# Performance work log

Measured on AMD Instinct MI355X. Metric: run time of the kernel, lower is better.

Reference implementation:

```python
import jax, jax.numpy as jnp
import numpy as np

N_NODES = 10000
N_EDGES = 160000
BATCH = 32
IN_FEAT = 64
POLY_K = 5
OUT_FEAT = 128


def setup_inputs() -> dict:
    key = jax.random.key(0)
    k_x, k_r, k_c, k_v, k_w, k_b = jax.random.split(key, 6)
    x = jax.random.normal(k_x, (BATCH, N_NODES, IN_FEAT), dtype=jnp.float32)
    lap_rows = jax.random.randint(k_r, (N_EDGES,), 0, N_NODES, dtype=jnp.int32)
    lap_cols = jax.random.randint(k_c, (N_EDGES,), 0, N_NODES, dtype=jnp.int32)
    # small values keep the degree-5 Chebyshev recurrence numerically tame
    lap_vals = jax.random.normal(k_v, (N_EDGES,), dtype=jnp.float32) * 0.05
    weight = jax.random.normal(k_w, (IN_FEAT * POLY_K, OUT_FEAT), dtype=jnp.float32) * 0.1
    bias = jax.random.normal(k_b, (1, 1, OUT_FEAT), dtype=jnp.float32) * 0.1
    return {"x": x, "lap_rows": lap_rows, "lap_cols": lap_cols,
            "lap_vals": lap_vals, "weight": weight, "bias": bias,
            "pooling_size": 4}


def _spmm(rows, cols, vals, m):
    # sparse [N,N] @ dense [N,M] via gather + segment_sum
    return jax.ops.segment_sum(vals[:, None] * m[cols], rows, num_segments=N_NODES)


def reference(x, lap_rows, lap_cols, lap_vals, weight, bias, pooling_size):
    B, N, F = x.shape
    K = POLY_K
    Fo = weight.shape[1]
    # x0: [N, F*B]
    x0 = jnp.transpose(x, (1, 2, 0)).reshape(N, F * B)
    terms = [x0]
    if K > 1:
        x1 = _spmm(lap_rows, lap_cols, lap_vals, x0)
        terms.append(x1)
        for _ in range(2, K):
            x2 = 2.0 * _spmm(lap_rows, lap_cols, lap_vals, x1) - x0
            terms.append(x2)
            x0, x1 = x1, x2
    xk = jnp.stack(terms, axis=0)                      # [K, N, F*B]
    xk = xk.reshape(K, N, F, B)
    xk = jnp.transpose(xk, (3, 1, 2, 0))               # [B, N, F, K]
    xk = xk.reshape(B * N, F * K)
    out = (xk @ weight).reshape(B, N, Fo)              # dense projection
    out = jax.nn.relu(out + bias)                      # bias + ReLU
    if pooling_size > 1:
        out = out.reshape(B, N // pooling_size, pooling_size, Fo).max(axis=2)
    return out
```

## Files before the change

### kernel.cpp

```cpp
#include <hip/hip_runtime.h>
#include <hip/hip_bf16.h>
#include <cstddef>
#include <cstdint>

#define N_NODES 10000
#define N_EDGES 160000
#define BATCH 32
#define IN_FEAT 64
#define POLY_K 5
#define OUT_FEAT 128
#define KTOT 320
#define POOLSZ 4
#define NPOOL 2500
#define NSL 16

typedef short bf16x8 __attribute__((ext_vector_type(8)));
typedef unsigned short u16x8 __attribute__((ext_vector_type(8)));
typedef unsigned int u32x4 __attribute__((ext_vector_type(4)));
typedef float f32x4 __attribute__((ext_vector_type(4)));
typedef float f32x2 __attribute__((ext_vector_type(2)));

__device__ __forceinline__ unsigned short f2bf(float f) {
  unsigned int u = __float_as_uint(f);
  unsigned int r = u + 0x7FFFu + ((u >> 16) & 1u);
  return (unsigned short)(r >> 16);
}
__device__ __forceinline__ float bf2f(unsigned short u) {
  return __uint_as_float(((unsigned int)u) << 16);
}
__device__ __forceinline__ f32x2 unpk(unsigned int u) {
  f32x2 r;
  r[0] = __uint_as_float(u << 16);
  r[1] = __uint_as_float(u & 0xFFFF0000u);
  return r;
}


__global__ void zero_int_kernel(int* __restrict__ p, int n) {
  int i = blockIdx.x * 256 + threadIdx.x;
  if (i < n) p[i] = 0;
}

__global__ void hist_kernel(const int* __restrict__ rows, int* __restrict__ deg) {
  int e = blockIdx.x * 256 + threadIdx.x;
  if (e < N_EDGES) atomicAdd(&deg[rows[e]], 1);
}

__global__ void scan_kernel(const int* __restrict__ deg, int* __restrict__ row_start,
                            int* __restrict__ cursor) {
  __shared__ int wsum[16];
  __shared__ int carry_sm;
  int t = threadIdx.x;
  int lane = t & 63, wid = t >> 6;
  if (t == 0) { carry_sm = 0; row_start[0] = 0; }
  __syncthreads();
  for (int base = 0; base < N_NODES; base += 1024) {
    int idx = base + t;
    int v = (idx < N_NODES) ? deg[idx] : 0;
    int x = v;
    #pragma unroll
    for (int off = 1; off < 64; off <<= 1) {
      int y = __shfl_up(x, off, 64);
      if (lane >= off) x += y;
    }
    if (lane == 63) wsum[wid] = x;
    __syncthreads();
    if (wid == 0) {
      int sv = (lane < 16) ? wsum[lane] : 0;
      #pragma unroll
      for (int off = 1; off < 16; off <<= 1) {
        int y = __shfl_up(sv, off, 64);
        if (lane >= off) sv += y;
      }
      if (lane < 16) wsum[lane] = sv;
    }
    __syncthreads();
    int incl = x + (wid > 0 ? wsum[wid - 1] : 0) + carry_sm;
    if (idx < N_NODES) {
      row_start[idx + 1] = incl;
      cursor[idx] = incl - v;
    }
    __syncthreads();
    if (t == 1023) carry_sm = incl;
    __syncthreads();
  }
}

__global__ void scatter_kernel(const int* __restrict__ rows, const int* __restrict__ cols,
                               const float* __restrict__ vals, int* __restrict__ cursor,
                               int* __restrict__ csr_cols, float* __restrict__ csr_vals) {
  int e = blockIdx.x * 256 + threadIdx.x;
  if (e < N_EDGES) {
    int r = rows[e];
    int p = atomicAdd(&cursor[r], 1);
    csr_cols[p] = cols[e];
    csr_vals[p] = vals[e];
  }
}


__global__ void wpack_kernel(const float* __restrict__ weight, unsigned short* __restrict__ wpack) {
  int id = blockIdx.x * 256 + threadIdx.x;
  if (id >= 5120) return;
  int ft = id / 640;
  int c = (id / 64) % 10;
  int l = id % 64;
  int fo = ft * 16 + (l & 15);
  unsigned short v[8];
  #pragma unroll
  for (int j = 0; j < 8; ++j) {
    int k = c * 32 + ((l >> 4)) * 8 + j;
    int row = (k & 63) * POLY_K + (k >> 6);
    v[j] = f2bf(weight[row * OUT_FEAT + fo]);
  }
  ushort4* dst = (ushort4*)&wpack[(size_t)id * 8];
  dst[0] = make_ushort4(v[0], v[1], v[2], v[3]);
  dst[1] = make_ushort4(v[4], v[5], v[6], v[7]);
}


template <int BB>
__global__ __launch_bounds__(256) void transpose_kernel(const float* __restrict__ x,
                                                        unsigned short* __restrict__ t0, int b0) {
  constexpr int CB = 64 * BB;
  constexpr int SCOLS = CB / NSL;
  constexpr size_t SLICE_SL = (size_t)N_NODES * SCOLS;
  int n = blockIdx.x;
  int t = threadIdx.x;
  for (int i = t * 8; i < CB; i += 2048) {
    int b = i >> 6;
    int f = i & 63;
    const float* xp = &x[((size_t)(b0 + b) * N_NODES + n) * IN_FEAT + f];
    float4 v0 = *(const float4*)xp;
    float4 v1 = *(const float4*)(xp + 4);
    u16x8 o;
    o[0] = f2bf(v0.x); o[1] = f2bf(v0.y); o[2] = f2bf(v0.z); o[3] = f2bf(v0.w);
    o[4] = f2bf(v1.x); o[5] = f2bf(v1.y); o[6] = f2bf(v1.z); o[7] = f2bf(v1.w);
    int sl = i / SCOLS;
    int cw = i & (SCOLS - 1);
    *(u16x8*)&t0[(size_t)sl * SLICE_SL + (size_t)n * SCOLS + cw] = o;
  }
}


template <int BB>
__global__ __launch_bounds__(256) void spmm_kernel(const unsigned short* __restrict__ xin,
                                                   const unsigned short* __restrict__ prev,
                                                   unsigned short* __restrict__ xout,
                                                   const int* __restrict__ row_start,
                                                   const int* __restrict__ csr_cols,
                                                   const float* __restrict__ csr_vals,
                                                   float alpha, int use_prev) {
  constexpr int CB = 64 * BB;
  constexpr int SCOLS = CB / NSL;
  constexpr size_t SLICE_SL = (size_t)N_NODES * SCOLS;
  constexpr int LPR = SCOLS / 8;
  constexpr int RPB = 256 / LPR;
  constexpr int RB = (N_NODES + RPB - 1) / RPB;
  constexpr int PHB = RB * 8;
  int bid = blockIdx.x;
  int phase = bid / PHB;
  int rem = bid - phase * PHB;
  int xcd = rem & 7;
  int rowblk = rem >> 3;
  int slice = phase * 8 + xcd;
  int t = threadIdx.x;
  int rl = t / LPR;
  int cl = t - rl * LPR;
  int n = rowblk * RPB + rl;
  if (n >= N_NODES) return;
  unsigned off = (unsigned)cl * 8u;

  const unsigned short* xs = xin  + (size_t)slice * SLICE_SL;
  const unsigned short* ps = prev + (size_t)slice * SLICE_SL;
  unsigned short*       os = xout + (size_t)slice * SLICE_SL;

  int s = row_start[n];
  int e = row_start[n + 1];
  f32x2 a0 = {0.f, 0.f}, a1 = {0.f, 0.f}, a2 = {0.f, 0.f}, a3 = {0.f, 0.f};

  int i = s;
  for (; i + 7 < e; i += 8) {
    int   c[8];
    float v[8];
    #pragma unroll
    for (int u = 0; u < 8; ++u) { c[u] = csr_cols[i + u]; v[u] = csr_vals[i + u]; }
    u32x4 d[8];
    #pragma unroll
    for (int u = 0; u < 8; ++u) d[u] = *(const u32x4*)&xs[(unsigned)c[u] * SCOLS + off];
    #pragma unroll
    for (int u = 0; u < 8; ++u) {
      f32x2 w = {v[u], v[u]};
      a0 = __builtin_elementwise_fma(w, unpk(d[u][0]), a0);
      a1 = __builtin_elementwise_fma(w, unpk(d[u][1]), a1);
      a2 = __builtin_elementwise_fma(w, unpk(d[u][2]), a2);
      a3 = __builtin_elementwise_fma(w, unpk(d[u][3]), a3);
    }
  }
  for (; i + 3 < e; i += 4) {
    int   c[4];
    float v[4];
    #pragma unroll
    for (int u = 0; u < 4; ++u) { c[u] = csr_cols[i + u]; v[u] = csr_vals[i + u]; }
    u32x4 d[4];
    #pragma unroll
    for (int u = 0; u < 4; ++u) d[u] = *(const u32x4*)&xs[(unsigned)c[u] * SCOLS + off];
    #pragma unroll
    for (int u = 0; u < 4; ++u) {
      f32x2 w = {v[u], v[u]};
      a0 = __builtin_elementwise_fma(w, unpk(d[u][0]), a0);
      a1 = __builtin_elementwise_fma(w, unpk(d[u][1]), a1);
      a2 = __builtin_elementwise_fma(w, unpk(d[u][2]), a2);
      a3 = __builtin_elementwise_fma(w, unpk(d[u][3]), a3);
    }
  }
  for (; i < e; ++i) {
    int c0 = csr_cols[i];
    float v0 = csr_vals[i];
    u32x4 d0 = *(const u32x4*)&xs[(unsigned)c0 * SCOLS + off];
    f32x2 w0 = {v0, v0};
    a0 = __builtin_elementwise_fma(w0, unpk(d0[0]), a0);
    a1 = __builtin_elementwise_fma(w0, unpk(d0[1]), a1);
    a2 = __builtin_elementwise_fma(w0, unpk(d0[2]), a2);
    a3 = __builtin_elementwise_fma(w0, unpk(d0[3]), a3);
  }

  unsigned nelt = (unsigned)n * SCOLS + off;
  u16x8 o;
  if (use_prev) {
    u32x4 qd = *(const u32x4*)&ps[nelt];
    f32x2 q0 = unpk(qd[0]), q1 = unpk(qd[1]), q2 = unpk(qd[2]), q3 = unpk(qd[3]);
    o[0] = f2bf(alpha * a0[0] - q0[0]); o[1] = f2bf(alpha * a0[1] - q0[1]);
    o[2] = f2bf(alpha * a1[0] - q1[0]); o[3] = f2bf(alpha * a1[1] - q1[1]);
    o[4] = f2bf(alpha * a2[0] - q2[0]); o[5] = f2bf(alpha * a2[1] - q2[1]);
    o[6] = f2bf(alpha * a3[0] - q3[0]); o[7] = f2bf(alpha * a3[1] - q3[1]);
  } else {
    o[0] = f2bf(alpha * a0[0]); o[1] = f2bf(alpha * a0[1]);
    o[2] = f2bf(alpha * a1[0]); o[3] = f2bf(alpha * a1[1]);
    o[4] = f2bf(alpha * a2[0]); o[5] = f2bf(alpha * a2[1]);
    o[6] = f2bf(alpha * a3[0]); o[7] = f2bf(alpha * a3[1]);
  }
  *(u16x8*)&os[nelt] = o;
}


template <int BB>
__global__ __launch_bounds__(256, 4) void gemm_mfma_kernel(const unsigned short* __restrict__ slices,
                                                           const unsigned short* __restrict__ wpack,
                                                           const float* __restrict__ bias,
                                                           float* __restrict__ out, int b0) {
  constexpr int CB = 64 * BB;
  constexpr int SCOLS = CB / NSL;
  constexpr size_t SLICE_SL = (size_t)N_NODES * SCOLS;
  constexpr int MB = (BB >= 16) ? 16 : BB;
  constexpr int MT = MB / 4;
  constexpr int SPAN = MB * 64;
  constexpr int ROWS = 4 * MB;
  __shared__ unsigned short A[ROWS * 320];

  int g = blockIdx.x;
  int bh = blockIdx.y;
  int t = threadIdx.x;

  constexpr int CHUNKS = ROWS * 40;
  for (int idx0 = 0; idx0 < CHUNKS; idx0 += 256) {
    int idx = idx0 + t;
    int row = idx / 40;
    int cphys = idx - row * 40;
    int clog = cphys ^ (row & 7);
    int kpoly = clog >> 3;
    int fb = (clog & 7) * 8;
    int bloc = row >> 2;
    int nd = row & 3;
    int c = bh * SPAN + bloc * 64 + fb;
    int sl = c / SCOLS;
    int cw = c & (SCOLS - 1);
    const unsigned short* gsrc = &slices[((size_t)kpoly * NSL + sl) * SLICE_SL +
                                         (size_t)(g * POOLSZ + nd) * SCOLS + cw];
    unsigned short* lbase = &A[(size_t)(idx0 + (t & 192)) * 8];
    __builtin_amdgcn_global_load_lds((const __attribute__((address_space(1))) unsigned int*)gsrc,
                                     (__attribute__((address_space(3))) unsigned int*)lbase,
                                     16, 0, 0);
  }
  __syncthreads();

  int w = t >> 6;
  int l = t & 63;
  int lm = l & 15;
  int q = l >> 4;
  int swz = lm & 7;

  f32x4 acc[MT][2];
  #pragma unroll
  for (int mt = 0; mt < MT; ++mt)
    #pragma unroll
    for (int fj = 0; fj < 2; ++fj) {
      acc[mt][fj][0] = 0.f; acc[mt][fj][1] = 0.f;
      acc[mt][fj][2] = 0.f; acc[mt][fj][3] = 0.f;
    }

  #pragma unroll
  for (int c = 0; c < 10; ++c) {
    bf16x8 bfrag[2];
    #pragma unroll
    for (int fj = 0; fj < 2; ++fj) {
      int fi = w * 2 + fj;
      bfrag[fj] = *(const bf16x8*)&wpack[(size_t)(((fi * 10) + c) * 64 + l) * 8];
    }
    #pragma unroll
    for (int mt = 0; mt < MT; ++mt) {
      bf16x8 afrag = *(const bf16x8*)&A[(mt * 16 + lm) * 320 + (((c * 4 + q) ^ swz) << 3)];
      acc[mt][0] = __builtin_amdgcn_mfma_f32_16x16x32_bf16(afrag, bfrag[0], acc[mt][0], 0, 0, 0);
      acc[mt][1] = __builtin_amdgcn_mfma_f32_16x16x32_bf16(afrag, bfrag[1], acc[mt][1], 0, 0, 0);
    }
  }

  #pragma unroll
  for (int fj = 0; fj < 2; ++fj) {
    int fo = (w * 2 + fj) * 16 + lm;
    float bv = bias[fo];
    #pragma unroll
    for (int mt = 0; mt < MT; ++mt) {
      float mx = fmaxf(fmaxf(acc[mt][fj][0], acc[mt][fj][1]),
                       fmaxf(acc[mt][fj][2], acc[mt][fj][3]));
      float val = fmaxf(mx + bv, 0.f);
      int b = b0 + bh * MB + mt * 4 + q;
      out[((size_t)b * NPOOL + g) * OUT_FEAT + fo] = val;
    }
  }
}


template <int BB>
static void run_pipeline(const float* x, const float* bias,
                         const int* row_start, const int* csr_cols, const float* csr_vals,
                         const unsigned short* wpack,
                         unsigned short* slices, float* out, hipStream_t stream) {
  constexpr int CB = 64 * BB;
  constexpr size_t TERM = (size_t)N_NODES * CB;
  constexpr int LPR = (CB / NSL) / 8;
  constexpr int RPB = 256 / LPR;
  constexpr int NBLK = ((N_NODES + RPB - 1) / RPB) * NSL;
  constexpr int MB = (BB >= 16) ? 16 : BB;
  for (int b0 = 0; b0 < BATCH; b0 += BB) {
    transpose_kernel<BB><<<N_NODES, 256, 0, stream>>>(x, slices, b0);
    for (int k = 1; k < POLY_K; ++k) {
      const unsigned short* xin  = slices + (size_t)(k - 1) * TERM;
      const unsigned short* prev = (k >= 2) ? slices + (size_t)(k - 2) * TERM : slices;
      unsigned short* xout = slices + (size_t)k * TERM;
      float alpha = (k == 1) ? 1.0f : 2.0f;
      spmm_kernel<BB><<<NBLK, 256, 0, stream>>>(xin, prev, xout, row_start,
                                                csr_cols, csr_vals, alpha,
                                                (k >= 2) ? 1 : 0);
    }
    gemm_mfma_kernel<BB><<<dim3(NPOOL, BB / MB), 256, 0, stream>>>(slices, wpack, bias, out, b0);
  }
}

static size_t needed_bytes(int BB) {
  return 1482112u + (size_t)6400000 * BB;
}

extern "C" void kernel_launch(void* const* d_in, const int* in_sizes, int n_in,
                              void* d_out, int out_size, void* d_ws, size_t ws_size,
                              hipStream_t stream) {
  const float* x        = (const float*)d_in[0];
  const int*   lap_rows = (const int*)d_in[1];
  const int*   lap_cols = (const int*)d_in[2];
  const float* lap_vals = (const float*)d_in[3];
  const float* weight   = (const float*)d_in[4];
  const float* bias     = (const float*)d_in[5];
  float* out = (float*)d_out;

  int* deg       = (int*)d_ws;
  int* cursor    = deg + 10016;
  int* row_start = cursor + 10016;
  int* csr_cols  = row_start + 10016;
  float* csr_vals = (float*)(csr_cols + N_EDGES);
  unsigned short* wpack = (unsigned short*)(csr_vals + N_EDGES);
  unsigned short* slices = wpack + 40960;

  int BB = 0;
  if      (ws_size >= needed_bytes(32)) BB = 32;
  else if (ws_size >= needed_bytes(16)) BB = 16;
  else if (ws_size >= needed_bytes(8))  BB = 8;
  else if (ws_size >= needed_bytes(4))  BB = 4;
  if (BB == 0) return;

  zero_int_kernel<<<(N_NODES + 255) / 256, 256, 0, stream>>>(deg, N_NODES);
  hist_kernel<<<(N_EDGES + 255) / 256, 256, 0, stream>>>(lap_rows, deg);
  scan_kernel<<<1, 1024, 0, stream>>>(deg, row_start, cursor);
  scatter_kernel<<<(N_EDGES + 255) / 256, 256, 0, stream>>>(lap_rows, lap_cols, lap_vals,
                                                            cursor, csr_cols, csr_vals);
  wpack_kernel<<<20, 256, 0, stream>>>(weight, wpack);

  switch (BB) {
    case 32: run_pipeline<32>(x, bias, row_start, csr_cols, csr_vals, wpack, slices, out, stream); break;
    case 16: run_pipeline<16>(x, bias, row_start, csr_cols, csr_vals, wpack, slices, out, stream); break;
    case 8:  run_pipeline<8>(x, bias, row_start, csr_cols, csr_vals, wpack, slices, out, stream); break;
    case 4:  run_pipeline<4>(x, bias, row_start, csr_cols, csr_vals, wpack, slices, out, stream); break;
  }
}
```

Before: 421.6 us.

## Interleave CSR col/val pairs and degree-sort rows within chunks for SpMM

Packs column index and value into one int2 array so each edge is fetched with a single 8-byte load instead of two separate loads. Adds a small kernel that insertion-sorts each 16-row chunk by degree and a permutation used by the SpMM kernel to map threads to rows. Rows with similar degree then share a wavefront, which is meant to reduce loop-trip divergence. The cost is an extra launch, a perm lookup per row, and a slightly larger workspace requirement.

```diff
diff --git a/kernel.cpp b/kernel.cpp
--- a/kernel.cpp
+++ b/kernel.cpp
@@ -88,14 +88,37 @@
 
 __global__ void scatter_kernel(const int* __restrict__ rows, const int* __restrict__ cols,
                                const float* __restrict__ vals, int* __restrict__ cursor,
-                               int* __restrict__ csr_cols, float* __restrict__ csr_vals) {
+                               int2* __restrict__ csr_pairs) {
   int e = blockIdx.x * 256 + threadIdx.x;
   if (e < N_EDGES) {
     int r = rows[e];
     int p = atomicAdd(&cursor[r], 1);
-    csr_cols[p] = cols[e];
-    csr_vals[p] = vals[e];
-  }
+    csr_pairs[p] = make_int2(cols[e], __float_as_int(vals[e]));
+  }
+}
+
+
+__global__ void bsort_kernel(const int* __restrict__ deg, int* __restrict__ perm) {
+  int chunk = blockIdx.x * 256 + threadIdx.x;
+  if (chunk >= (N_NODES + 15) / 16) return;
+  int base = chunk * 16;
+  int idx[16], dg[16];
+  #pragma unroll
+  for (int j = 0; j < 16; ++j) {
+    int r = base + j;
+    idx[j] = r;
+    dg[j] = (r < N_NODES) ? deg[r] : 0x7fffffff;
+  }
+  #pragma unroll
+  for (int a = 1; a < 16; ++a) {
+    int dv = dg[a], iv = idx[a];
+    int b = a - 1;
+    while (b >= 0 && dg[b] > dv) { dg[b + 1] = dg[b]; idx[b + 1] = idx[b]; --b; }
+    dg[b + 1] = dv; idx[b + 1] = iv;
+  }
+  #pragma unroll
+  for (int j = 0; j < 16; ++j)
+    if (base + j < N_NODES) perm[base + j] = idx[j];
 }
 
 
@@ -148,8 +171,8 @@
                                                    const unsigned short* __restrict__ prev,
                                                    unsigned short* __restrict__ xout,
                                                    const int* __restrict__ row_start,
-                                                   const int* __restrict__ csr_cols,
-                                                   const float* __restrict__ csr_vals,
+                                                   const int2* __restrict__ csr_pairs,
+                                                   const int* __restrict__ perm,
                                                    float alpha, int use_prev) {
   constexpr int CB = 64 * BB;
   constexpr int SCOLS = CB / NSL;
@@ -167,8 +190,9 @@
   int t = threadIdx.x;
   int rl = t / LPR;
   int cl = t - rl * LPR;
-  int n = rowblk * RPB + rl;
-  if (n >= N_NODES) return;
+  int si = rowblk * RPB + rl;
+  if (si >= N_NODES) return;
+  int n = perm[si];
   unsigned off = (unsigned)cl * 8u;
 
   const unsigned short* xs = xin  + (size_t)slice * SLICE_SL;
@@ -181,16 +205,16 @@
 
   int i = s;
   for (; i + 7 < e; i += 8) {
-    int   c[8];
-    float v[8];
-    #pragma unroll
-    for (int u = 0; u < 8; ++u) { c[u] = csr_cols[i + u]; v[u] = csr_vals[i + u]; }
+    int2 E[8];
+    #pragma unroll
+    for (int u = 0; u < 8; ++u) E[u] = csr_pairs[i + u];
     u32x4 d[8];
     #pragma unroll
-    for (int u = 0; u < 8; ++u) d[u] = *(const u32x4*)&xs[(unsigned)c[u] * SCOLS + off];
+    for (int u = 0; u < 8; ++u) d[u] = *(const u32x4*)&xs[(unsigned)E[u].x * SCOLS + off];
     #pragma unroll
     for (int u = 0; u < 8; ++u) {
-      f32x2 w = {v[u], v[u]};
+      float vv = __int_as_float(E[u].y);
+      f32x2 w = {vv, vv};
       a0 = __builtin_elementwise_fma(w, unpk(d[u][0]), a0);
       a1 = __builtin_elementwise_fma(w, unpk(d[u][1]), a1);
       a2 = __builtin_elementwise_fma(w, unpk(d[u][2]), a2);
@@ -198,16 +222,16 @@
     }
   }
   for (; i + 3 < e; i += 4) {
-    int   c[4];
-    float v[4];
-    #pragma unroll
-    for (int u = 0; u < 4; ++u) { c[u] = csr_cols[i + u]; v[u] = csr_vals[i + u]; }
+    int2 E[4];
+    #pragma unroll
+    for (int u = 0; u < 4; ++u) E[u] = csr_pairs[i + u];
     u32x4 d[4];
     #pragma unroll
-    for (int u = 0; u < 4; ++u) d[u] = *(const u32x4*)&xs[(unsigned)c[u] * SCOLS + off];
+    for (int u = 0; u < 4; ++u) d[u] = *(const u32x4*)&xs[(unsigned)E[u].x * SCOLS + off];
     #pragma unroll
     for (int u = 0; u < 4; ++u) {
-      f32x2 w = {v[u], v[u]};
+      float vv = __int_as_float(E[u].y);
+      f32x2 w = {vv, vv};
       a0 = __builtin_elementwise_fma(w, unpk(d[u][0]), a0);
       a1 = __builtin_elementwise_fma(w, unpk(d[u][1]), a1);
       a2 = __builtin_elementwise_fma(w, unpk(d[u][2]), a2);
@@ -215,10 +239,10 @@
     }
   }
   for (; i < e; ++i) {
-    int c0 = csr_cols[i];
-    float v0 = csr_vals[i];
-    u32x4 d0 = *(const u32x4*)&xs[(unsigned)c0 * SCOLS + off];
-    f32x2 w0 = {v0, v0};
+    int2 E0 = csr_pairs[i];
+    u32x4 d0 = *(const u32x4*)&xs[(unsigned)E0.x * SCOLS + off];
+    float vv = __int_as_float(E0.y);
+    f32x2 w0 = {vv, vv};
     a0 = __builtin_elementwise_fma(w0, unpk(d0[0]), a0);
     a1 = __builtin_elementwise_fma(w0, unpk(d0[1]), a1);
     a2 = __builtin_elementwise_fma(w0, unpk(d0[2]), a2);
@@ -333,7 +357,7 @@
 
 template <int BB>
 static void run_pipeline(const float* x, const float* bias,
-                         const int* row_start, const int* csr_cols, const float* csr_vals,
+                         const int* row_start, const int2* csr_pairs, const int* perm,
                          const unsigned short* wpack,
                          unsigned short* slices, float* out, hipStream_t stream) {
   constexpr int CB = 64 * BB;
@@ -350,7 +374,7 @@
       unsigned short* xout = slices + (size_t)k * TERM;
       float alpha = (k == 1) ? 1.0f : 2.0f;
       spmm_kernel<BB><<<NBLK, 256, 0, stream>>>(xin, prev, xout, row_start,
-                                                csr_cols, csr_vals, alpha,
+                                                csr_pairs, perm, alpha,
                                                 (k >= 2) ? 1 : 0);
     }
     gemm_mfma_kernel<BB><<<dim3(NPOOL, BB / MB), 256, 0, stream>>>(slices, wpack, bias, out, b0);
@@ -358,7 +382,7 @@
 }
 
 static size_t needed_bytes(int BB) {
-  return 1482112u + (size_t)6400000 * BB;
+  return 1522176u + (size_t)6400000 * BB;
 }
 
 extern "C" void kernel_launch(void* const* d_in, const int* in_sizes, int n_in,
@@ -375,9 +399,9 @@
   int* deg       = (int*)d_ws;
   int* cursor    = deg + 10016;
   int* row_start = cursor + 10016;
-  int* csr_cols  = row_start + 10016;
-  float* csr_vals = (float*)(csr_cols + N_EDGES);
-  unsigned short* wpack = (unsigned short*)(csr_vals + N_EDGES);
+  int* perm      = row_start + 10016;
+  int2* csr_pairs = (int2*)(perm + 10016);
+  unsigned short* wpack = (unsigned short*)(csr_pairs + N_EDGES);
   unsigned short* slices = wpack + 40960;
 
   int BB = 0;
@@ -391,13 +415,14 @@
   hist_kernel<<<(N_EDGES + 255) / 256, 256, 0, stream>>>(lap_rows, deg);
   scan_kernel<<<1, 1024, 0, stream>>>(deg, row_start, cursor);
   scatter_kernel<<<(N_EDGES + 255) / 256, 256, 0, stream>>>(lap_rows, lap_cols, lap_vals,
-                                                            cursor, csr_cols, csr_vals);
+                                                            cursor, csr_pairs);
+  bsort_kernel<<<3, 256, 0, stream>>>(deg, perm);
   wpack_kernel<<<20, 256, 0, stream>>>(weight, wpack);
 
   switch (BB) {
-    case 32: run_pipeline<32>(x, bias, row_start, csr_cols, csr_vals, wpack, slices, out, stream); break;
-    case 16: run_pipeline<16>(x, bias, row_start, csr_cols, csr_vals, wpack, slices, out, stream); break;
-    case 8:  run_pipeline<8>(x, bias, row_start, csr_cols, csr_vals, wpack, slices, out, stream); break;
-    case 4:  run_pipeline<4>(x, bias, row_start, csr_cols, csr_vals, wpack, slices, out, stream); break;
-  }
-}
+    case 32: run_pipeline<32>(x, bias, row_start, csr_pairs, perm, wpack, slices, out, stream); break;
+    case 16: run_pipeline<16>(x, bias, row_start, csr_pairs, perm, wpack, slices, out, stream); break;
+    case 8:  run_pipeline<8>(x, bias, row_start, csr_pairs, perm, wpack, slices, out, stream); break;
+    case 4:  run_pipeline<4>(x, bias, row_start, csr_pairs, perm, wpack, slices, out, stream); break;
+  }
+}
```

Result: no change. 424.5 us (+0.7%).
